# Kernel tuning notes

Measured on AMD Instinct MI355X. Metric: run time of the kernel, lower is better.

Reference implementation:

```python
import jax, jax.numpy as jnp
import numpy as np

NUM_HEADS = 16
DIM = 2048
SEQ = 2048
ROPE_BASE = 10000.0
EPS = 1.1920929e-07  # torch.finfo(float32).eps, F.rms_norm default


def rms_norm(x):
    return x * jax.lax.rsqrt(jnp.mean(x * x, axis=-1, keepdims=True) + EPS)


def rotary(x):
    # x: [B, T, H, Dh]; rotate halves with per-position freqs
    B, T, H, Dh = x.shape
    inv_freq = (1.0 / ROPE_BASE) ** (jnp.arange(0, Dh, 2, dtype=jnp.float32) / Dh)
    freqs = jnp.arange(T, dtype=jnp.float32)[:, None] * inv_freq[None, :]  # [T, Dh/2]
    cos = jnp.cos(freqs)[None, :, None, :]
    sin = jnp.sin(freqs)[None, :, None, :]
    x1, x2 = jnp.split(x, 2, axis=-1)
    y1 = x1 * cos + x2 * sin
    y2 = -x1 * sin + x2 * cos
    return jnp.concatenate([y1, y2], axis=-1).astype(x.dtype)


def setup_inputs() -> dict:
    key = jax.random.key(0)
    ks = jax.random.split(key, 7)
    s = 1.0 / np.sqrt(DIM)
    return {
        "x": jax.random.normal(ks[0], (1, SEQ, DIM), dtype=jnp.float32),
        "vi": jax.random.normal(ks[1], (1, SEQ, DIM), dtype=jnp.float32),
        "wq": jax.random.normal(ks[2], (DIM, DIM), dtype=jnp.float32) * s,
        "wk": jax.random.normal(ks[3], (DIM, DIM), dtype=jnp.float32) * s,
        "wv": jax.random.normal(ks[4], (DIM, DIM), dtype=jnp.float32) * s,
        "wproj": jax.random.normal(ks[5], (DIM, DIM), dtype=jnp.float32) * s,
        "lambdas": jax.random.uniform(ks[6], (2,), dtype=jnp.float32),
    }


def reference(x, vi, wq, wk, wv, wproj, lambdas):
    B, T, D = x.shape
    H = NUM_HEADS
    Dh = D // H
    # CastedLinear: F.linear(x, W) == x @ W.T, no bias
    q = (x @ wq.T).reshape(B, T, H, Dh)
    k = (x @ wk.T).reshape(B, T, H, Dh)
    v = (x @ wv.T).reshape(B, T, H, Dh)
    v = lambdas[0] * v + lambdas[1] * vi.reshape(B, T, H, Dh)
    q, k = rms_norm(q), rms_norm(k)
    q, k = rotary(q), rotary(k)
    # causal attention (block_mask in source is causal), scale = 1/sqrt(Dh)
    scores = jnp.einsum("bthd,bshd->bhts", q, k) / jnp.sqrt(jnp.float32(Dh))
    causal = jnp.tril(jnp.ones((T, T), dtype=bool))
    scores = jnp.where(causal[None, None, :, :], scores, jnp.float32(-1e30))
    attn = jax.nn.softmax(scores, axis=-1)
    y = jnp.einsum("bhts,bshd->bthd", attn, v).reshape(B, T, D)
    return y @ wproj.T
```

## Files before the change

### kernel.cpp

```cpp
#include <hip/hip_runtime.h>

#define TSEQ 2048
#define DM   2048
#define NHEAD 16

typedef __bf16 bf16x8 __attribute__((ext_vector_type(8)));
typedef float  f32x4  __attribute__((ext_vector_type(4)));
typedef unsigned short ushort8v __attribute__((ext_vector_type(8)));
typedef unsigned int u32x4v __attribute__((ext_vector_type(4)));
typedef const __attribute__((address_space(1))) void* gas_cvp;
typedef __attribute__((address_space(3))) void* las_vp;

__device__ __forceinline__ unsigned short f2bf(float f) {
  unsigned int u = __builtin_bit_cast(unsigned int, f);
  u += 0x7FFFu + ((u >> 16) & 1u);
  return (unsigned short)(u >> 16);
}

__global__ __launch_bounds__(256) void cvt_bf16(const float* __restrict__ in,
                                                unsigned short* __restrict__ out,
                                                int n8) {
  int i = blockIdx.x * 256 + threadIdx.x;
  if (i >= n8) return;
  const float4* p = (const float4*)in + (size_t)i * 2;
  float4 a = p[0], b = p[1];
  ushort8v o;
  o[0] = f2bf(a.x); o[1] = f2bf(a.y); o[2] = f2bf(a.z); o[3] = f2bf(a.w);
  o[4] = f2bf(b.x); o[5] = f2bf(b.y); o[6] = f2bf(b.z); o[7] = f2bf(b.w);
  *((ushort8v*)out + i) = o;
}

template<int BM>
__global__ __launch_bounds__(512, 2) void gemm8p(const unsigned short* __restrict__ A,
                                                 const unsigned short* __restrict__ B,
                                                 float* __restrict__ C,
                                                 int N) {
  constexpr int ABYTES = BM * 128;
  constexpr int ACH = ABYTES / 8192;
  constexpr int SCH = ACH + 4;
  constexpr int MFR = BM / 32;
  __shared__ char lds[2 * ABYTES + 2 * 32768];

  const char* Ag = (const char*)A;
  const char* Bg = (const char*)B;

  int nwg = gridDim.x;
  int cpx = nwg >> 3;
  int orig = blockIdx.x;
  int swz = (orig & 7) * cpx + (orig >> 3);
  int nbx = N >> 8;
  int bx = swz % nbx, by = swz / nbx;
  int tileM = by * BM, tileN = bx * 256;

  int tid = threadIdx.x;
  int w = tid >> 6, lane = tid & 63;
  int l15 = lane & 15, l4 = lane >> 4;
  int wm = w >> 2, wn = w & 3;
  int xorsw = (l15 & 7) << 4;

  f32x4 acc[MFR][4] = {};
  bf16x8 a[4][2], b0[2][2], b1[2][2];

  auto stage = [&](int i, int kt, int bsel) {
    char* dst;
    const char* src;
    if (i < ACH) {
      int L = (i * 512 + tid) * 16;
      int row = L >> 7, colb = L & 127;
      dst = lds + bsel * ABYTES + L;
      src = Ag + (size_t)(tileM + row) * 4096 + kt * 128 + (colb ^ ((row & 7) << 4));
    } else {
      int L = ((i - ACH) * 512 + tid) * 16;
      int row = L >> 7, colb = L & 127;
      dst = lds + 2 * ABYTES + bsel * 32768 + L;
      src = Bg + (size_t)(tileN + row) * 4096 + kt * 128 + (colb ^ ((row & 7) << 4));
    }
    __builtin_amdgcn_global_load_lds((gas_cvp)src, (las_vp)dst, 16, 0, 0);
  };
  auto readA = [&](int ah, const char* Ab) {
    #pragma unroll
    for (int mfl = 0; mfl < 4; ++mfl)
      #pragma unroll
      for (int kk = 0; kk < 2; ++kk) {
        int row = wm * (BM / 2) + (ah * 4 + mfl) * 16 + l15;
        a[mfl][kk] = *(const bf16x8*)(Ab + row * 128 + ((kk * 64 + l4 * 16) ^ xorsw));
      }
  };
  auto readB = [&](bf16x8 (&bb)[2][2], int bh, const char* Bb) {
    #pragma unroll
    for (int nfl = 0; nfl < 2; ++nfl)
      #pragma unroll
      for (int kk = 0; kk < 2; ++kk) {
        int row = wn * 64 + (bh * 2 + nfl) * 16 + l15;
        bb[nfl][kk] = *(const bf16x8*)(Bb + row * 128 + ((kk * 64 + l4 * 16) ^ xorsw));
      }
  };
  auto mfma16 = [&](int ah, int bh, bf16x8 (&bb)[2][2]) {
    __builtin_amdgcn_s_setprio(1);
    #pragma unroll
    for (int mfl = 0; mfl < 4; ++mfl)
      #pragma unroll
      for (int nfl = 0; nfl < 2; ++nfl)
        #pragma unroll
        for (int kk = 0; kk < 2; ++kk)
          acc[ah * 4 + mfl][bh * 2 + nfl] =
            __builtin_amdgcn_mfma_f32_16x16x32_bf16(a[mfl][kk], bb[nfl][kk],
                                                    acc[ah * 4 + mfl][bh * 2 + nfl], 0, 0, 0);
    __builtin_amdgcn_s_setprio(0);
  };

  #pragma unroll
  for (int i = 0; i < SCH; ++i) stage(i, 0, 0);

  #pragma unroll 2
  for (int t = 0; t < 32; ++t) {
    int buf = t & 1;
    const char* Ab = lds + buf * ABYTES;
    const char* Bb = lds + 2 * ABYTES + buf * 32768;
    bool pf = (t + 1 < 32);

    asm volatile("s_waitcnt vmcnt(0)" ::: "memory");
    __builtin_amdgcn_s_barrier();
    asm volatile("" ::: "memory");

    if constexpr (BM == 256) {
      readA(0, Ab); readB(b0, 0, Bb);
      if (pf) { stage(0, t + 1, buf ^ 1); stage(1, t + 1, buf ^ 1);
                stage(2, t + 1, buf ^ 1); stage(3, t + 1, buf ^ 1); }
      __builtin_amdgcn_s_barrier();
      mfma16(0, 0, b0);
      __builtin_amdgcn_s_barrier();
      readB(b1, 1, Bb);
      if (pf) { stage(4, t + 1, buf ^ 1); stage(5, t + 1, buf ^ 1);
                stage(6, t + 1, buf ^ 1); stage(7, t + 1, buf ^ 1); }
      __builtin_amdgcn_s_barrier();
      mfma16(0, 1, b1);
      __builtin_amdgcn_s_barrier();
      readA(1, Ab);
      __builtin_amdgcn_s_barrier();
      mfma16(1, 1, b1);
      __builtin_amdgcn_s_barrier();
      mfma16(1, 0, b0);
      __builtin_amdgcn_s_barrier();
    } else {
      readA(0, Ab); readB(b0, 0, Bb);
      if (pf) { stage(0, t + 1, buf ^ 1); stage(1, t + 1, buf ^ 1);
                stage(2, t + 1, buf ^ 1); stage(3, t + 1, buf ^ 1);
                stage(4, t + 1, buf ^ 1); stage(5, t + 1, buf ^ 1); }
      __builtin_amdgcn_s_barrier();
      mfma16(0, 0, b0);
      __builtin_amdgcn_s_barrier();
      readB(b1, 1, Bb);
      __builtin_amdgcn_s_barrier();
      mfma16(0, 1, b1);
      __builtin_amdgcn_s_barrier();
    }
  }

  #pragma unroll
  for (int mf = 0; mf < MFR; ++mf) {
    int r0 = tileM + wm * (BM / 2) + mf * 16 + l4 * 4;
    #pragma unroll
    for (int nf = 0; nf < 4; ++nf) {
      int c0 = tileN + wn * 64 + nf * 16 + l15;
      #pragma unroll
      for (int j = 0; j < 4; ++j)
        C[(size_t)(r0 + j) * N + c0] = acc[mf][nf][j];
    }
  }
}

__global__ __launch_bounds__(256) void qkv_post(const float* __restrict__ qkv,
                                                const float* __restrict__ vi,
                                                const float* __restrict__ lam,
                                                unsigned short* __restrict__ qb,
                                                unsigned short* __restrict__ kb,
                                                unsigned short* __restrict__ vb) {
  int wid = blockIdx.x * 4 + (threadIdx.x >> 6);
  int lane = threadIdx.x & 63;
  int t = wid >> 4, h = wid & 15;
  const float* base = qkv + (size_t)t * (3 * DM) + h * 128;
  float l0 = lam[0], l1 = lam[1];

  float invf = exp2f((float)lane * -0.20762050593046014f);
  float ang = (float)t * invf;
  float sn, cs;
  sincosf(ang, &sn, &cs);

  size_t ob = (size_t)t * DM + h * 128;
  {
    float a = base[lane], b = base[lane + 64];
    float ss = a * a + b * b;
    #pragma unroll
    for (int m = 1; m < 64; m <<= 1) ss += __shfl_xor(ss, m, 64);
    float sc = rsqrtf(ss * (1.0f / 128.0f) + 1.1920929e-07f);
    a *= sc; b *= sc;
    qb[ob + lane]      = f2bf(a * cs + b * sn);
    qb[ob + 64 + lane] = f2bf(b * cs - a * sn);
  }
  {
    float a = base[2048 + lane], b = base[2048 + 64 + lane];
    float ss = a * a + b * b;
    #pragma unroll
    for (int m = 1; m < 64; m <<= 1) ss += __shfl_xor(ss, m, 64);
    float sc = rsqrtf(ss * (1.0f / 128.0f) + 1.1920929e-07f);
    a *= sc; b *= sc;
    kb[ob + lane]      = f2bf(a * cs + b * sn);
    kb[ob + 64 + lane] = f2bf(b * cs - a * sn);
  }
  {
    const float* vib = vi + (size_t)t * DM + h * 128;
    vb[ob + lane]      = f2bf(l0 * base[4096 + lane]      + l1 * vib[lane]);
    vb[ob + 64 + lane] = f2bf(l0 * base[4096 + 64 + lane] + l1 * vib[lane + 64]);
  }
}

__global__ __launch_bounds__(256) void transpose_v(const unsigned short* __restrict__ vb,
                                                   unsigned short* __restrict__ vbT) {
  __shared__ __align__(16) unsigned short tile[64][68];
  int t0 = blockIdx.x * 64, d0 = blockIdx.y * 64, h = blockIdx.z;
  int tid = threadIdx.x;
  int li = tid >> 4;
  int lj = (tid & 15) * 4;
  #pragma unroll
  for (int p = 0; p < 4; ++p) {
    int i = p * 16 + li;
    ushort4 v = *(const ushort4*)(vb + (size_t)(t0 + i) * DM + h * 128 + d0 + lj);
    tile[i][lj] = v.x; tile[i][lj + 1] = v.y; tile[i][lj + 2] = v.z; tile[i][lj + 3] = v.w;
  }
  __syncthreads();
  #pragma unroll
  for (int p = 0; p < 4; ++p) {
    int j = p * 16 + li;
    ushort4 wv;
    wv.x = tile[lj][j]; wv.y = tile[lj + 1][j]; wv.z = tile[lj + 2][j]; wv.w = tile[lj + 3][j];
    *(ushort4*)(vbT + (size_t)h * 128 * TSEQ + (size_t)(d0 + j) * TSEQ + t0 + lj) = wv;
  }
}

__global__ __launch_bounds__(256, 2) void attn_split(const unsigned short* __restrict__ qb,
                                                     const unsigned short* __restrict__ kb,
                                                     const unsigned short* __restrict__ vbT,
                                                     float* __restrict__ Opart,
                                                     float2* __restrict__ ml) {
  __shared__ __align__(16) char Ks[2][16384];
  __shared__ __align__(16) char Vs[2][16384];

  int bi = blockIdx.x;
  int qblk = 15 - (bi >> 5);
  int h = (bi >> 1) & 15;
  int s = bi & 1;
  int half = qblk + 1;
  int st0 = s ? half : 0;
  int st1 = s ? 2 * half : half;

  int tid = threadIdx.x, w = tid >> 6, lane = tid & 63;
  int l15 = lane & 15, l4 = lane >> 4;
  int qr0 = qblk * 128 + w * 32;
  int xorK = (l15 & 7) << 4;
  int srcA = ((((l4 << 1)) & 3) * 16 + l15) << 2;
  int srcB = ((((l4 << 1) + 1) & 3) * 16 + l15) << 2;
  bool hi4 = (l4 >> 1) != 0;

  bf16x8 q_frag[2][4];
  #pragma unroll
  for (int qt = 0; qt < 2; ++qt) {
    const unsigned short* qrow = qb + (size_t)(qr0 + qt * 16 + l15) * DM + h * 128 + l4 * 8;
    #pragma unroll
    for (int kk = 0; kk < 4; ++kk) q_frag[qt][kk] = *(const bf16x8*)(qrow + kk * 32);
  }

  const char* kbase = (const char*)kb + (size_t)h * 256;
  const char* vbase = (const char*)vbT + (size_t)h * 128 * TSEQ * 2;

  f32x4 acc_o[2][8] = {};
  float mrow[2] = {-1e30f, -1e30f};
  float lrow[2] = {0.f, 0.f};
  const float scale = 0.08838834764831845f;

  auto stage = [&](int st, int bsel) {
    const char* kb1 = kbase + (size_t)st * 64 * 4096;
    const char* vb1 = vbase + (size_t)st * 64 * 2;
    #pragma unroll
    for (int it = 0; it < 4; ++it) {
      int L = (it * 256 + tid) * 16;
      int row = L >> 8, b = L & 255;
      const char* src = kb1 + (size_t)row * 4096 + (b ^ ((row & 7) << 4));
      __builtin_amdgcn_global_load_lds((gas_cvp)src, (las_vp)(&Ks[bsel][0] + L), 16, 0, 0);
    }
    #pragma unroll
    for (int it = 0; it < 4; ++it) {
      int L = (it * 256 + tid) * 16;
      int row = L >> 7, b = L & 127;
      const char* src = vb1 + (size_t)row * (TSEQ * 2) + (b ^ ((row & 7) << 4));
      __builtin_amdgcn_global_load_lds((gas_cvp)src, (las_vp)(&Vs[bsel][0] + L), 16, 0, 0);
    }
  };

  stage(st0, 0);
  int buf = 0;

  for (int st = st0; st < st1; ++st) {
    asm volatile("s_waitcnt vmcnt(0) lgkmcnt(0)" ::: "memory");
    __builtin_amdgcn_s_barrier();
    __builtin_amdgcn_sched_barrier(0);
    if (st + 1 < st1) stage(st + 1, buf ^ 1);

    f32x4 acc_s[2][4] = {};
    __builtin_amdgcn_s_setprio(1);
    #pragma unroll
    for (int j = 0; j < 4; ++j) {
      const char* kr = &Ks[buf][0] + (j * 16 + l15) * 256;
      #pragma unroll
      for (int kk = 0; kk < 4; ++kk) {
        bf16x8 kf = *(const bf16x8*)(kr + ((l4 * 16 + kk * 64) ^ xorK));
        acc_s[0][j] = __builtin_amdgcn_mfma_f32_16x16x32_bf16(kf, q_frag[0][kk], acc_s[0][j], 0, 0, 0);
        acc_s[1][j] = __builtin_amdgcn_mfma_f32_16x16x32_bf16(kf, q_frag[1][kk], acc_s[1][j], 0, 0, 0);
      }
    }
    __builtin_amdgcn_s_setprio(0);

    int kv0 = st * 64;
    bool needmask = (kv0 + 63) > qr0;
    u32x4v pf[2][2];

    #pragma unroll
    for (int qt = 0; qt < 2; ++qt) {
      int qg = qr0 + qt * 16 + l15;
      float sv[4][4];
      float pmax = -1e30f;
      if (needmask) {
        #pragma unroll
        for (int j = 0; j < 4; ++j)
          #pragma unroll
          for (int r = 0; r < 4; ++r) {
            float v = acc_s[qt][j][r] * scale;
            if ((kv0 + j * 16 + l4 * 4 + r) > qg) v = -1e30f;
            sv[j][r] = v;
            pmax = fmaxf(pmax, v);
          }
      } else {
        #pragma unroll
        for (int j = 0; j < 4; ++j)
          #pragma unroll
          for (int r = 0; r < 4; ++r) {
            float v = acc_s[qt][j][r] * scale;
            sv[j][r] = v;
            pmax = fmaxf(pmax, v);
          }
      }
      pmax = fmaxf(pmax, __shfl_xor(pmax, 16, 64));
      pmax = fmaxf(pmax, __shfl_xor(pmax, 32, 64));
      float mn = fmaxf(mrow[qt], pmax);
      float f = __expf(mrow[qt] - mn);
      mrow[qt] = mn;

      float psum = 0.f;
      unsigned pk[4][2];
      #pragma unroll
      for (int j = 0; j < 4; ++j)
        #pragma unroll
        for (int rr = 0; rr < 2; ++rr) {
          float p0 = __expf(sv[j][2 * rr] - mn);
          float p1 = __expf(sv[j][2 * rr + 1] - mn);
          psum += p0 + p1;
          pk[j][rr] = (unsigned)f2bf(p0) | ((unsigned)f2bf(p1) << 16);
        }
      psum += __shfl_xor(psum, 16, 64);
      psum += __shfl_xor(psum, 32, 64);
      lrow[qt] = lrow[qt] * f + psum;
      #pragma unroll
      for (int n = 0; n < 8; ++n) acc_o[qt][n] *= f;

      #pragma unroll
      for (int kk = 0; kk < 2; ++kk) {
        u32x4v pw;
        #pragma unroll
        for (int w2 = 0; w2 < 4; ++w2) {
          int rr = w2 & 1;
          int src = (w2 < 2) ? srcA : srcB;
          unsigned c0 = (unsigned)__builtin_amdgcn_ds_bpermute(src, (int)pk[2 * kk][rr]);
          unsigned c1 = (unsigned)__builtin_amdgcn_ds_bpermute(src, (int)pk[2 * kk + 1][rr]);
          pw[w2] = hi4 ? c1 : c0;
        }
        pf[qt][kk] = pw;
      }
    }

    __builtin_amdgcn_s_setprio(1);
    #pragma unroll
    for (int kk = 0; kk < 2; ++kk) {
      bf16x8 pb0 = __builtin_bit_cast(bf16x8, pf[0][kk]);
      bf16x8 pb1 = __builtin_bit_cast(bf16x8, pf[1][kk]);
      #pragma unroll
      for (int n = 0; n < 8; ++n) {
        bf16x8 vf = *(const bf16x8*)(&Vs[buf][0] + (n * 16 + l15) * 128 + ((kk * 64 + l4 * 16) ^ xorK));
        acc_o[0][n] = __builtin_amdgcn_mfma_f32_16x16x32_bf16(vf, pb0, acc_o[0][n], 0, 0, 0);
        acc_o[1][n] = __builtin_amdgcn_mfma_f32_16x16x32_bf16(vf, pb1, acc_o[1][n], 0, 0, 0);
      }
    }
    __builtin_amdgcn_s_setprio(0);
    buf ^= 1;
  }

  float* Op = Opart + (size_t)s * (TSEQ * DM);
  #pragma unroll
  for (int qt = 0; qt < 2; ++qt) {
    int q = qr0 + qt * 16 + l15;
    #pragma unroll
    for (int n = 0; n < 8; ++n)
      *(f32x4*)(Op + (size_t)q * DM + h * 128 + n * 16 + l4 * 4) = acc_o[qt][n];
    if (l4 == 0)
      ml[(size_t)s * (TSEQ * NHEAD) + (size_t)q * NHEAD + h] = make_float2(mrow[qt], lrow[qt]);
  }
}

__global__ __launch_bounds__(256) void attn_combine(const float* __restrict__ Opart,
                                                    const float2* __restrict__ ml,
                                                    unsigned short* __restrict__ yb) {
  int idx = blockIdx.x * 256 + threadIdx.x;
  int rowid = idx >> 5;
  float2 ml0 = ml[rowid];
  float2 ml1 = ml[TSEQ * NHEAD + rowid];
  float m = fmaxf(ml0.x, ml1.x);
  float a0 = __expf(ml0.x - m), a1 = __expf(ml1.x - m);
  float inv = 1.0f / (a0 * ml0.y + a1 * ml1.y);
  float4 o0 = ((const float4*)Opart)[idx];
  float4 o1 = ((const float4*)(Opart + (size_t)TSEQ * DM))[idx];
  ushort4 r;
  r.x = f2bf((a0 * o0.x + a1 * o1.x) * inv);
  r.y = f2bf((a0 * o0.y + a1 * o1.y) * inv);
  r.z = f2bf((a0 * o0.z + a1 * o1.z) * inv);
  r.w = f2bf((a0 * o0.w + a1 * o1.w) * inv);
  *(ushort4*)(yb + (size_t)idx * 4) = r;
}

extern "C" void kernel_launch(void* const* d_in, const int* in_sizes, int n_in,
                              void* d_out, int out_size, void* d_ws, size_t ws_size,
                              hipStream_t stream) {
  const float* x   = (const float*)d_in[0];
  const float* vi  = (const float*)d_in[1];
  const float* wq  = (const float*)d_in[2];
  const float* wk  = (const float*)d_in[3];
  const float* wv  = (const float*)d_in[4];
  const float* wp  = (const float*)d_in[5];
  const float* lam = (const float*)d_in[6];

  const size_t MB = 1024 * 1024;
  const int NEL = DM * TSEQ;
  const int N8  = NEL / 8;
  char* ws = (char*)d_ws;
  unsigned short* xb    = (unsigned short*)(ws);
  unsigned short* wqkvb = (unsigned short*)(ws + 8  * MB);
  unsigned short* wpb   = (unsigned short*)(ws + 32 * MB);
  float*          qkv32 = (float*)(ws + 40 * MB);
  float*          Opart = (float*)(ws + 40 * MB);
  float2*         mlbuf = (float2*)(ws + 72 * MB);
  unsigned short* qb2   = (unsigned short*)(ws + 88 * MB);
  unsigned short* kb2   = (unsigned short*)(ws + 96 * MB);
  unsigned short* vb    = (unsigned short*)(ws + 104 * MB);
  unsigned short* vbT   = (unsigned short*)(ws + 112 * MB);
  unsigned short* yb    = (unsigned short*)(ws + 120 * MB);

  cvt_bf16<<<N8 / 256, 256, 0, stream>>>(x,  xb, N8);
  cvt_bf16<<<N8 / 256, 256, 0, stream>>>(wq, wqkvb,                  N8);
  cvt_bf16<<<N8 / 256, 256, 0, stream>>>(wk, wqkvb + (size_t)NEL,     N8);
  cvt_bf16<<<N8 / 256, 256, 0, stream>>>(wv, wqkvb + (size_t)2 * NEL, N8);
  cvt_bf16<<<N8 / 256, 256, 0, stream>>>(wp, wpb, N8);

  gemm8p<256><<<192, 512, 0, stream>>>(xb, wqkvb, qkv32, 3 * DM);

  qkv_post<<<(TSEQ * NHEAD) / 4, 256, 0, stream>>>(qkv32, vi, lam, qb2, kb2, vb);

  transpose_v<<<dim3(TSEQ / 64, 2, NHEAD), 256, 0, stream>>>(vb, vbT);

  attn_split<<<512, 256, 0, stream>>>(qb2, kb2, vbT, Opart, mlbuf);
  attn_combine<<<(TSEQ * DM / 4) / 256, 256, 0, stream>>>(Opart, mlbuf, yb);

  gemm8p<128><<<128, 512, 0, stream>>>(yb, wpb, (float*)d_out, DM);
}
```

Measured before the change: 199.5 us.

## Replace shared GEMM template with tuned QKV and split-K projection GEMMs

Replaces the templated 8-wave GEMM with two dedicated kernels. The QKV GEMM uses 128x192 tiles with 4 waves and 512 workgroups to better fill the CUs, loading a whole K-step before one MFMA burst. The output projection uses 128x128 tiles with intra-workgroup split-K across wave pairs, a 3-stage LDS pipeline, and an LDS reduction at the end, so 256 workgroups are launched instead of 128. This trades larger LDS use and an extra reduction step for more parallelism and deeper prefetch.

Result: faster. 189.3 us (-5.1%).

```diff
diff --git a/kernel.cpp b/kernel.cpp
--- a/kernel.cpp
+++ b/kernel.cpp
@@ -30,142 +30,174 @@
   *((ushort8v*)out + i) = o;
 }
 
-template<int BM>
-__global__ __launch_bounds__(512, 2) void gemm8p(const unsigned short* __restrict__ A,
-                                                 const unsigned short* __restrict__ B,
-                                                 float* __restrict__ C,
-                                                 int N) {
-  constexpr int ABYTES = BM * 128;
-  constexpr int ACH = ABYTES / 8192;
-  constexpr int SCH = ACH + 4;
-  constexpr int MFR = BM / 32;
-  __shared__ char lds[2 * ABYTES + 2 * 32768];
+__global__ __launch_bounds__(256, 2) void gemm_qkv(const unsigned short* __restrict__ A,
+                                                   const unsigned short* __restrict__ B,
+                                                   float* __restrict__ C) {
+  constexpr int TB = (128 + 192) * 128;
+  __shared__ char lds[2 * TB];
+
+  int orig = blockIdx.x;
+  int swz = (orig & 7) * 64 + (orig >> 3);
+  int bx = swz & 31, by = swz >> 5;
+  int tileM = by * 128, tileN = bx * 192;
+
+  int tid = threadIdx.x, w = tid >> 6, lane = tid & 63;
+  int l15 = lane & 15, l4 = lane >> 4;
+  int wm = w >> 1, wn = w & 1;
+  int xorsw = (l15 & 7) << 4;
+  int srow = tid >> 3, scolb = (tid & 7) * 16;
 
   const char* Ag = (const char*)A;
   const char* Bg = (const char*)B;
 
-  int nwg = gridDim.x;
-  int cpx = nwg >> 3;
-  int orig = blockIdx.x;
-  int swz = (orig & 7) * cpx + (orig >> 3);
-  int nbx = N >> 8;
-  int bx = swz % nbx, by = swz / nbx;
-  int tileM = by * BM, tileN = bx * 256;
-
-  int tid = threadIdx.x;
-  int w = tid >> 6, lane = tid & 63;
-  int l15 = lane & 15, l4 = lane >> 4;
-  int wm = w >> 2, wn = w & 3;
-  int xorsw = (l15 & 7) << 4;
-
-  f32x4 acc[MFR][4] = {};
-  bf16x8 a[4][2], b0[2][2], b1[2][2];
-
-  auto stage = [&](int i, int kt, int bsel) {
-    char* dst;
-    const char* src;
-    if (i < ACH) {
-      int L = (i * 512 + tid) * 16;
-      int row = L >> 7, colb = L & 127;
-      dst = lds + bsel * ABYTES + L;
-      src = Ag + (size_t)(tileM + row) * 4096 + kt * 128 + (colb ^ ((row & 7) << 4));
-    } else {
-      int L = ((i - ACH) * 512 + tid) * 16;
-      int row = L >> 7, colb = L & 127;
-      dst = lds + 2 * ABYTES + bsel * 32768 + L;
-      src = Bg + (size_t)(tileN + row) * 4096 + kt * 128 + (colb ^ ((row & 7) << 4));
-    }
-    __builtin_amdgcn_global_load_lds((gas_cvp)src, (las_vp)dst, 16, 0, 0);
+  f32x4 acc[4][6] = {};
+
+  auto stage = [&](int kt, int bsel) {
+    char* dst0 = lds + bsel * TB + srow * 128 + scolb;
+    #pragma unroll
+    for (int i = 0; i < 10; ++i) {
+      int row = i * 32 + srow;
+      const char* src = (row < 128 ? Ag + (size_t)(tileM + row) * 4096
+                                   : Bg + (size_t)(tileN + row - 128) * 4096)
+                        + kt * 128 + (scolb ^ ((row & 7) << 4));
+      __builtin_amdgcn_global_load_lds((gas_cvp)src, (las_vp)(dst0 + i * 4096), 16, 0, 0);
+    }
   };
-  auto readA = [&](int ah, const char* Ab) {
-    #pragma unroll
-    for (int mfl = 0; mfl < 4; ++mfl)
-      #pragma unroll
-      for (int kk = 0; kk < 2; ++kk) {
-        int row = wm * (BM / 2) + (ah * 4 + mfl) * 16 + l15;
-        a[mfl][kk] = *(const bf16x8*)(Ab + row * 128 + ((kk * 64 + l4 * 16) ^ xorsw));
-      }
-  };
-  auto readB = [&](bf16x8 (&bb)[2][2], int bh, const char* Bb) {
-    #pragma unroll
-    for (int nfl = 0; nfl < 2; ++nfl)
-      #pragma unroll
-      for (int kk = 0; kk < 2; ++kk) {
-        int row = wn * 64 + (bh * 2 + nfl) * 16 + l15;
-        bb[nfl][kk] = *(const bf16x8*)(Bb + row * 128 + ((kk * 64 + l4 * 16) ^ xorsw));
-      }
-  };
-  auto mfma16 = [&](int ah, int bh, bf16x8 (&bb)[2][2]) {
-    __builtin_amdgcn_s_setprio(1);
-    #pragma unroll
-    for (int mfl = 0; mfl < 4; ++mfl)
-      #pragma unroll
-      for (int nfl = 0; nfl < 2; ++nfl)
-        #pragma unroll
-        for (int kk = 0; kk < 2; ++kk)
-          acc[ah * 4 + mfl][bh * 2 + nfl] =
-            __builtin_amdgcn_mfma_f32_16x16x32_bf16(a[mfl][kk], bb[nfl][kk],
-                                                    acc[ah * 4 + mfl][bh * 2 + nfl], 0, 0, 0);
-    __builtin_amdgcn_s_setprio(0);
-  };
-
-  #pragma unroll
-  for (int i = 0; i < SCH; ++i) stage(i, 0, 0);
-
+
+  stage(0, 0);
   #pragma unroll 2
   for (int t = 0; t < 32; ++t) {
     int buf = t & 1;
-    const char* Ab = lds + buf * ABYTES;
-    const char* Bb = lds + 2 * ABYTES + buf * 32768;
-    bool pf = (t + 1 < 32);
-
     asm volatile("s_waitcnt vmcnt(0)" ::: "memory");
     __builtin_amdgcn_s_barrier();
-    asm volatile("" ::: "memory");
-
-    if constexpr (BM == 256) {
-      readA(0, Ab); readB(b0, 0, Bb);
-      if (pf) { stage(0, t + 1, buf ^ 1); stage(1, t + 1, buf ^ 1);
-                stage(2, t + 1, buf ^ 1); stage(3, t + 1, buf ^ 1); }
-      __builtin_amdgcn_s_barrier();
-      mfma16(0, 0, b0);
-      __builtin_amdgcn_s_barrier();
-      readB(b1, 1, Bb);
-      if (pf) { stage(4, t + 1, buf ^ 1); stage(5, t + 1, buf ^ 1);
-                stage(6, t + 1, buf ^ 1); stage(7, t + 1, buf ^ 1); }
-      __builtin_amdgcn_s_barrier();
-      mfma16(0, 1, b1);
-      __builtin_amdgcn_s_barrier();
-      readA(1, Ab);
-      __builtin_amdgcn_s_barrier();
-      mfma16(1, 1, b1);
-      __builtin_amdgcn_s_barrier();
-      mfma16(1, 0, b0);
-      __builtin_amdgcn_s_barrier();
-    } else {
-      readA(0, Ab); readB(b0, 0, Bb);
-      if (pf) { stage(0, t + 1, buf ^ 1); stage(1, t + 1, buf ^ 1);
-                stage(2, t + 1, buf ^ 1); stage(3, t + 1, buf ^ 1);
-                stage(4, t + 1, buf ^ 1); stage(5, t + 1, buf ^ 1); }
-      __builtin_amdgcn_s_barrier();
-      mfma16(0, 0, b0);
-      __builtin_amdgcn_s_barrier();
-      readB(b1, 1, Bb);
-      __builtin_amdgcn_s_barrier();
-      mfma16(0, 1, b1);
-      __builtin_amdgcn_s_barrier();
-    }
+    __builtin_amdgcn_sched_barrier(0);
+    if (t + 1 < 32) stage(t + 1, buf ^ 1);
+
+    const char* Lb = lds + buf * TB;
+    bf16x8 a[4][2], b[6][2];
+    #pragma unroll
+    for (int mf = 0; mf < 4; ++mf)
+      #pragma unroll
+      for (int kk = 0; kk < 2; ++kk)
+        a[mf][kk] = *(const bf16x8*)(Lb + (wm * 64 + mf * 16 + l15) * 128 + ((kk * 64 + l4 * 16) ^ xorsw));
+    #pragma unroll
+    for (int nf = 0; nf < 6; ++nf)
+      #pragma unroll
+      for (int kk = 0; kk < 2; ++kk)
+        b[nf][kk] = *(const bf16x8*)(Lb + (128 + wn * 96 + nf * 16 + l15) * 128 + ((kk * 64 + l4 * 16) ^ xorsw));
+    asm volatile("s_waitcnt lgkmcnt(0)" ::: "memory");
+    __builtin_amdgcn_sched_barrier(0);
+    __builtin_amdgcn_s_setprio(1);
+    #pragma unroll
+    for (int kk = 0; kk < 2; ++kk)
+      #pragma unroll
+      for (int mf = 0; mf < 4; ++mf)
+        #pragma unroll
+        for (int nf = 0; nf < 6; ++nf)
+          acc[mf][nf] = __builtin_amdgcn_mfma_f32_16x16x32_bf16(a[mf][kk], b[nf][kk], acc[mf][nf], 0, 0, 0);
+    __builtin_amdgcn_s_setprio(0);
   }
 
   #pragma unroll
-  for (int mf = 0; mf < MFR; ++mf) {
-    int r0 = tileM + wm * (BM / 2) + mf * 16 + l4 * 4;
-    #pragma unroll
-    for (int nf = 0; nf < 4; ++nf) {
-      int c0 = tileN + wn * 64 + nf * 16 + l15;
+  for (int mf = 0; mf < 4; ++mf) {
+    int r0 = tileM + wm * 64 + mf * 16 + l4 * 4;
+    #pragma unroll
+    for (int nf = 0; nf < 6; ++nf) {
+      int c0 = tileN + wn * 96 + nf * 16 + l15;
       #pragma unroll
       for (int j = 0; j < 4; ++j)
-        C[(size_t)(r0 + j) * N + c0] = acc[mf][nf][j];
+        C[(size_t)(r0 + j) * 6144 + c0] = acc[mf][nf][j];
+    }
+  }
+}
+
+__global__ __launch_bounds__(512, 2) void gemm_proj(const unsigned short* __restrict__ A,
+                                                    const unsigned short* __restrict__ B,
+                                                    float* __restrict__ C) {
+  constexpr int TB = 256 * 128;
+  __shared__ char lds[3 * TB];
+
+  int orig = blockIdx.x;
+  int swz = (orig & 7) * 32 + (orig >> 3);
+  int bx = swz & 15, by = swz >> 4;
+  int tileM = by * 128, tileN = bx * 128;
+
+  int tid = threadIdx.x, w = tid >> 6, lane = tid & 63;
+  int l15 = lane & 15, l4 = lane >> 4;
+  int wm = w >> 2, wn = (w >> 1) & 1, ks = w & 1;
+  int xorsw = (l15 & 7) << 4;
+  int srow = tid >> 3, scolb = (tid & 7) * 16;
+  int kb = ks * 64;
+
+  const char* Ag = (const char*)A;
+  const char* Bg = (const char*)B;
+
+  f32x4 acc[4][4] = {};
+
+  auto stage = [&](int kt, int bsel) {
+    char* dst0 = lds + bsel * TB + srow * 128 + scolb;
+    #pragma unroll
+    for (int i = 0; i < 4; ++i) {
+      int row = i * 64 + srow;
+      const char* src = (row < 128 ? Ag + (size_t)(tileM + row) * 4096
+                                   : Bg + (size_t)(tileN + row - 128) * 4096)
+                        + kt * 128 + (scolb ^ ((row & 7) << 4));
+      __builtin_amdgcn_global_load_lds((gas_cvp)src, (las_vp)(dst0 + i * 8192), 16, 0, 0);
+    }
+  };
+
+  stage(0, 0);
+  stage(1, 1);
+  #pragma unroll 3
+  for (int t = 0; t < 32; ++t) {
+    int buf = t % 3;
+    if (t + 1 < 32) { asm volatile("s_waitcnt vmcnt(4)" ::: "memory"); }
+    else            { asm volatile("s_waitcnt vmcnt(0)" ::: "memory"); }
+    __builtin_amdgcn_s_barrier();
+    __builtin_amdgcn_sched_barrier(0);
+    if (t + 2 < 32) stage(t + 2, (t + 2) % 3);
+
+    const char* Lb = lds + buf * TB;
+    bf16x8 a[4], b[4];
+    #pragma unroll
+    for (int mf = 0; mf < 4; ++mf)
+      a[mf] = *(const bf16x8*)(Lb + (wm * 64 + mf * 16 + l15) * 128 + ((kb + l4 * 16) ^ xorsw));
+    #pragma unroll
+    for (int nf = 0; nf < 4; ++nf)
+      b[nf] = *(const bf16x8*)(Lb + (128 + wn * 64 + nf * 16 + l15) * 128 + ((kb + l4 * 16) ^ xorsw));
+    asm volatile("s_waitcnt lgkmcnt(0)" ::: "memory");
+    __builtin_amdgcn_sched_barrier(0);
+    __builtin_amdgcn_s_setprio(1);
+    #pragma unroll
+    for (int mf = 0; mf < 4; ++mf)
+      #pragma unroll
+      for (int nf = 0; nf < 4; ++nf)
+        acc[mf][nf] = __builtin_amdgcn_mfma_f32_16x16x32_bf16(a[mf], b[nf], acc[mf][nf], 0, 0, 0);
+    __builtin_amdgcn_s_setprio(0);
+  }
+
+  __syncthreads();
+  int pair = w >> 1;
+  if (ks == 1) {
+    #pragma unroll
+    for (int mf = 0; mf < 4; ++mf)
+      #pragma unroll
+      for (int nf = 0; nf < 4; ++nf)
+        *(f32x4*)(lds + pair * 16384 + ((mf * 4 + nf) * 64 + lane) * 16) = acc[mf][nf];
+  }
+  __syncthreads();
+  if (ks == 0) {
+    #pragma unroll
+    for (int mf = 0; mf < 4; ++mf) {
+      int r0 = tileM + wm * 64 + mf * 16 + l4 * 4;
+      #pragma unroll
+      for (int nf = 0; nf < 4; ++nf) {
+        f32x4 o = acc[mf][nf] + *(const f32x4*)(lds + pair * 16384 + ((mf * 4 + nf) * 64 + lane) * 16);
+        int c0 = tileN + wn * 64 + nf * 16 + l15;
+        #pragma unroll
+        for (int j = 0; j < 4; ++j)
+          C[(size_t)(r0 + j) * 2048 + c0] = o[j];
+      }
     }
   }
 }
@@ -468,7 +500,7 @@
   cvt_bf16<<<N8 / 256, 256, 0, stream>>>(wv, wqkvb + (size_t)2 * NEL, N8);
   cvt_bf16<<<N8 / 256, 256, 0, stream>>>(wp, wpb, N8);
 
-  gemm8p<256><<<192, 512, 0, stream>>>(xb, wqkvb, qkv32, 3 * DM);
+  gemm_qkv<<<512, 256, 0, stream>>>(xb, wqkvb, qkv32);
 
   qkv_post<<<(TSEQ * NHEAD) / 4, 256, 0, stream>>>(qkv32, vi, lam, qb2, kb2, vb);
 
@@ -477,5 +509,5 @@
   attn_split<<<512, 256, 0, stream>>>(qb2, kb2, vbT, Opart, mlbuf);
   attn_combine<<<(TSEQ * DM / 4) / 256, 256, 0, stream>>>(Opart, mlbuf, yb);
 
-  gemm8p<128><<<128, 512, 0, stream>>>(yb, wpb, (float*)d_out, DM);
-}
+  gemm_proj<<<256, 512, 0, stream>>>(yb, wpb, (float*)d_out);
+}
```
